# Kernel optimization log

Measured on AMD Instinct MI355X. Metric: run time of the kernel, lower is better.

Reference implementation:

```python
import jax, jax.numpy as jnp
import numpy as np

B, C_IN, C_OUT, H, W = 16, 192, 192, 128, 128
K_EXPERTS, LATENT_DIM = 8, 64


def setup_inputs() -> dict:
    key = jax.random.key(0)
    ks = jax.random.split(key, 6)
    s = lambda fan: np.float32(1.0 / np.sqrt(fan))
    return {
        "x": jax.random.normal(ks[0], (B, C_IN, H, W), jnp.float32),
        "latent": jax.random.normal(ks[1], (B, LATENT_DIM), jnp.float32),
        # DyConv2d: K expert 3x3 kernels + biases, attention FC from latent
        "expert_w": jax.random.normal(ks[2], (K_EXPERTS, C_OUT, C_IN, 3, 3), jnp.float32) * s(C_IN * 9),
        "expert_b": jnp.zeros((K_EXPERTS, C_OUT), jnp.float32),
        "attn_w": jax.random.normal(ks[3], (K_EXPERTS, LATENT_DIM), jnp.float32) * s(LATENT_DIM),
        "attn_b": jnp.zeros((K_EXPERTS,), jnp.float32),
        # static conv2 (3x3) weights
        "conv2_w": jax.random.normal(ks[4], (C_OUT, C_OUT, 3, 3), jnp.float32) * s(C_OUT * 9),
        "conv2_b": jnp.zeros((C_OUT,), jnp.float32),
    }


def _conv3x3(x, w, b):
    # x: [N,C,H,W], w: [O,I,3,3] -> [N,O,H,W]
    y = jax.lax.conv_general_dilated(
        x, w, window_strides=(1, 1), padding=((1, 1), (1, 1)),
        dimension_numbers=("NCHW", "OIHW", "NCHW"))
    return y + b[None, :, None, None]


def reference(x, latent, expert_w, expert_b, attn_w, attn_b, conv2_w, conv2_b):
    identity = x  # stride=1, in_ch==out_ch -> adaptor is None
    # ---- DyConv2d: latent -> expert attention -> per-sample kernel ----
    attn = jax.nn.softmax(latent @ attn_w.T + attn_b, axis=-1)        # [B,K]
    w_dyn = jnp.einsum("bk,koihw->boihw", attn, expert_w)            # [B,O,I,3,3]
    b_dyn = attn @ expert_b                                          # [B,O]
    # per-sample conv, vectorized over batch
    out = jax.vmap(lambda xi, wi, bi: _conv3x3(xi[None], wi, bi)[0])(x, w_dyn, b_dyn)
    out = jax.nn.silu(out)
    # ---- static conv3x3 ----
    out = _conv3x3(out, conv2_w, conv2_b)
    out = jax.nn.silu(out)
    return out + identity
```

## Files before the change

### kernel.cpp

```cpp
#include <hip/hip_runtime.h>
#include <stdint.h>

typedef __bf16 bf16;
typedef bf16 bf16x8 __attribute__((ext_vector_type(8)));
typedef bf16 bf16x4 __attribute__((ext_vector_type(4)));
typedef float f32x4 __attribute__((ext_vector_type(4)));

#define B_   16
#define CI   192
#define CO   192
#define H_   128
#define W_   128
#define KE   8
#define LD   64
#define KTOT 1728
#define HP   130
#define HPHP (HP*HP)
#define NPX  (H_*W_)
#define NT   54

__device__ __forceinline__ void gll16(const void* g, void* l) {
  __builtin_amdgcn_global_load_lds(
      (const __attribute__((address_space(1))) unsigned int*)g,
      (__attribute__((address_space(3))) unsigned int*)l, 16, 0, 0);
}

__device__ __forceinline__ float silu_f(float x) {
  return x / (1.f + __expf(-x));
}

__global__ void k_attn(const float* __restrict__ latent, const float* __restrict__ attn_w,
                       const float* __restrict__ attn_b, float* __restrict__ attn) {
  int t = threadIdx.x;
  int b = t >> 3, k = t & 7;
  float s = attn_b[k];
  for (int d = 0; d < LD; ++d) s += latent[b*LD + d] * attn_w[k*LD + d];
  float m = s;
  for (int off = 4; off; off >>= 1) m = fmaxf(m, __shfl_xor(m, off, 8));
  float e = __expf(s - m);
  float sum = e;
  for (int off = 4; off; off >>= 1) sum += __shfl_xor(sum, off, 8);
  attn[t] = e / sum;
}

__global__ void k_bdyn(const float* __restrict__ attn, const float* __restrict__ expert_b,
                       float* __restrict__ bdyn) {
  int j = blockIdx.x * 256 + threadIdx.x;
  if (j >= B_ * CO) return;
  int b = j / CO, o = j - b * CO;
  float s = 0.f;
  #pragma unroll
  for (int e = 0; e < KE; ++e) s += attn[b*KE + e] * expert_b[e*CO + o];
  bdyn[j] = s;
}

__global__ void k_wdyn(const float* __restrict__ expert_w, const float* __restrict__ attn,
                       bf16* __restrict__ w_re) {
  int o = blockIdx.x;
  int chunk = o >> 4, row = o & 15, c = (row >> 1) & 3;
  __shared__ float ew[KE][KTOT];
  __shared__ float al[B_][KE];
  for (int e = 0; e < KE; ++e)
    for (int j = threadIdx.x; j < KTOT; j += 256)
      ew[e][j] = expert_w[((size_t)e*CO + o)*KTOT + j];
  if (threadIdx.x < B_*KE) al[threadIdx.x >> 3][threadIdx.x & 7] = attn[threadIdx.x];
  __syncthreads();
  for (int idx = threadIdx.x; idx < B_*KTOT; idx += 256) {
    int b = idx / KTOT, k = idx - b*KTOT;
    int rs = k / 192, i = k - rs*192;
    float s = 0.f;
    #pragma unroll
    for (int e = 0; e < KE; ++e) s += al[b][e] * ew[e][i*9 + rs];
    int kt = k >> 5, kslot = (k >> 3) & 3, j = k & 7;
    int slot = row*4 + (kslot ^ c);
    w_re[((((size_t)b*NT + kt)*12 + chunk)*64 + slot)*8 + j] = (bf16)s;
  }
}

__global__ void k_w2re(const float* __restrict__ conv2_w, bf16* __restrict__ w2_re) {
  int o = blockIdx.x;
  int chunk = o >> 4, row = o & 15, c = (row >> 1) & 3;
  __shared__ float cw[KTOT];
  for (int j = threadIdx.x; j < KTOT; j += 256) cw[j] = conv2_w[(size_t)o*KTOT + j];
  __syncthreads();
  for (int k = threadIdx.x; k < KTOT; k += 256) {
    int rs = k / 192, i = k - rs*192;
    int kt = k >> 5, kslot = (k >> 3) & 3, j = k & 7;
    int slot = row*4 + (kslot ^ c);
    w2_re[(((size_t)kt*12 + chunk)*64 + slot)*8 + j] = (bf16)cw[i*9 + rs];
  }
}

__global__ void k_xpack(const float* __restrict__ x, bf16* __restrict__ xpack) {
  int h2 = blockIdx.x, ib = blockIdx.y, b = blockIdx.z;
  size_t rowbase = (((size_t)b*24 + ib)*HP + h2)*HP;
  int t = threadIdx.x;
  if (h2 == 0 || h2 == HP-1) {
    uint4 z = make_uint4(0,0,0,0);
    for (int w = t; w < HP; w += 128) *(uint4*)(xpack + (rowbase + w)*8) = z;
    return;
  }
  __shared__ float tt[8][128];
  int h = h2 - 1;
  #pragma unroll
  for (int ii = 0; ii < 8; ++ii)
    tt[ii][t] = x[(((size_t)b*CI + ib*8 + ii)*H_ + h)*W_ + t];
  __syncthreads();
  bf16x8 v;
  #pragma unroll
  for (int ii = 0; ii < 8; ++ii) v[ii] = (bf16)tt[ii][t];
  *(bf16x8*)(xpack + (rowbase + t + 1)*8) = v;
  if (t == 0) {
    uint4 z = make_uint4(0,0,0,0);
    *(uint4*)(xpack + rowbase*8) = z;
    *(uint4*)(xpack + (rowbase + HP-1)*8) = z;
  }
}

__global__ void k_midborder(bf16* __restrict__ midpack) {
  int bi = blockIdx.x;
  size_t base = (size_t)bi * HPHP;
  uint4 z = make_uint4(0,0,0,0);
  for (int j = threadIdx.x; j < 516; j += 256) {
    int h2, w2;
    if (j < 130)      { h2 = 0;       w2 = j; }
    else if (j < 260) { h2 = 129;     w2 = j - 130; }
    else if (j < 388) { h2 = j - 259; w2 = 0; }
    else              { h2 = j - 387; w2 = 129; }
    *(uint4*)(midpack + (base + (size_t)h2*HP + w2)*8) = z;
  }
}

template<int MODE>
__global__ __launch_bounds__(256, 2)
void k_conv(const bf16* __restrict__ wre, const bf16* __restrict__ inpack,
            const float* __restrict__ bias_g, const float* __restrict__ xin,
            bf16* __restrict__ outpack, float* __restrict__ outp) {
  const int tid  = threadIdx.x;
  const int lane = tid & 63;
  const int wv   = tid >> 6;
  const int wm   = wv >> 1;
  const int wn   = wv & 1;
  const int l15  = lane & 15, l4 = lane >> 4;

  const int bid  = blockIdx.x;
  const int n    = (bid & 7) * 128 + (bid >> 3);
  const int b    = n >> 6;
  const int tile = n & 63;
  const int p0   = tile * 256;
  const int h0   = tile * 2;

  __shared__ __align__(16) bf16 Alds[2][12*512];
  __shared__ __align__(16) bf16 Blds[3][16*512];
  __shared__ float bias_lds[CO];

  if (tid < CO) bias_lds[tid] = (MODE == 0) ? bias_g[b*CO + tid] : bias_g[tid];

  const size_t wbase = (MODE == 0) ? ((size_t)b*CO*KTOT) : 0;

  const bf16* aS = wre + wbase + (size_t)wv*512 + lane*8;
  const bf16* bS[4];
  #pragma unroll
  for (int c = 0; c < 4; ++c)
    bS[c] = inpack + ((((size_t)b*24 + wv)*HP + h0 + (c >> 1))*HP + (c & 1)*64 + lane)*8;

  int rsn = 0, ibn = 0, boff = 0;
  auto badv = [&]() {
    if (++ibn == 6) {
      ibn = 0; ++rsn;
      boff += (((rsn % 3) == 0) ? (HP - 2) : 1) * 8 - 20*HPHP*8;
    } else {
      boff += 4*HPHP*8;
    }
  };

  f32x4 acc[6][8];
  #pragma unroll
  for (int mf = 0; mf < 6; ++mf)
    #pragma unroll
    for (int nf = 0; nf < 8; ++nf)
      #pragma unroll
      for (int jj = 0; jj < 4; ++jj) acc[mf][nf][jj] = 0.f;

  const int sw = l15*4 + (l4 ^ ((l15 >> 1) & 3));

  {
    #pragma unroll
    for (int c = 0; c < 3; ++c) gll16(aS + c*2048, &Alds[0][(wv + c*4)*512]);
    aS += 6144;
    #pragma unroll
    for (int c = 0; c < 4; ++c) gll16(bS[c] + boff, &Blds[0][(wv*4 + c)*512]);
    badv();
    #pragma unroll
    for (int c = 0; c < 4; ++c) gll16(bS[c] + boff, &Blds[1][(wv*4 + c)*512]);
    badv();
  }

  int bcur = 0, bnxt = 2;
  for (int t = 0; t < NT; ++t) {
    if (t < NT-1) asm volatile("s_waitcnt vmcnt(4)" ::: "memory");
    else          asm volatile("s_waitcnt vmcnt(0)" ::: "memory");
    asm volatile("s_barrier" ::: "memory");

    const bf16* A  = Alds[t & 1];
    const bf16* Bp = Blds[bcur];

    bf16x8 af0 = *(const bf16x8*)(A + (wm*6 + 0)*512 + sw*8);
    bf16x8 af1 = *(const bf16x8*)(A + (wm*6 + 1)*512 + sw*8);
    bf16x8 af2 = *(const bf16x8*)(A + (wm*6 + 2)*512 + sw*8);
    bf16x8 af3 = *(const bf16x8*)(A + (wm*6 + 3)*512 + sw*8);
    bf16x8 af4 = *(const bf16x8*)(A + (wm*6 + 4)*512 + sw*8);
    bf16x8 af5 = *(const bf16x8*)(A + (wm*6 + 5)*512 + sw*8);

    if (t + 1 < NT) {
      bf16* An = (bf16*)Alds[(t+1) & 1];
      #pragma unroll
      for (int c = 0; c < 3; ++c) gll16(aS + c*2048, An + (wv + c*4)*512);
      aS += 6144;
    }
    if (t + 2 < NT) {
      bf16* Bn = (bf16*)Blds[bnxt];
      #pragma unroll
      for (int c = 0; c < 4; ++c) gll16(bS[c] + boff, Bn + (wv*4 + c)*512);
      badv();
    }

    __builtin_amdgcn_s_setprio(1);
    #pragma unroll
    for (int nf = 0; nf < 8; ++nf) {
      bf16x8 bv = *(const bf16x8*)(Bp + (size_t)(l4*256 + wn*128 + nf*16 + l15)*8);
      acc[0][nf] = __builtin_amdgcn_mfma_f32_16x16x32_bf16(af0, bv, acc[0][nf], 0, 0, 0);
      acc[1][nf] = __builtin_amdgcn_mfma_f32_16x16x32_bf16(af1, bv, acc[1][nf], 0, 0, 0);
      acc[2][nf] = __builtin_amdgcn_mfma_f32_16x16x32_bf16(af2, bv, acc[2][nf], 0, 0, 0);
      acc[3][nf] = __builtin_amdgcn_mfma_f32_16x16x32_bf16(af3, bv, acc[3][nf], 0, 0, 0);
      acc[4][nf] = __builtin_amdgcn_mfma_f32_16x16x32_bf16(af4, bv, acc[4][nf], 0, 0, 0);
      acc[5][nf] = __builtin_amdgcn_mfma_f32_16x16x32_bf16(af5, bv, acc[5][nf], 0, 0, 0);
    }
    __builtin_amdgcn_s_setprio(0);

    bcur = (bcur == 2) ? 0 : bcur + 1;
    bnxt = (bnxt == 2) ? 0 : bnxt + 1;
  }

  #pragma unroll
  for (int mf = 0; mf < 6; ++mf) {
    int ob = wm*96 + mf*16 + l4*4;
    #pragma unroll
    for (int nf = 0; nf < 8; ++nf) {
      int pl = wn*128 + nf*16 + l15;
      int p  = p0 + pl;
      f32x4 v = acc[mf][nf];
      if (MODE == 0) {
        int h = p >> 7, w = p & 127;
        bf16x4 pk;
        #pragma unroll
        for (int jj = 0; jj < 4; ++jj) {
          float xv = v[jj] + bias_lds[ob + jj];
          pk[jj] = (bf16)silu_f(xv);
        }
        size_t basep = (((size_t)b*24 + (ob >> 3))*HP + (h + 1))*HP + (w + 1);
        *(bf16x4*)(outpack + basep*8 + (ob & 7)) = pk;
      } else {
        #pragma unroll
        for (int jj = 0; jj < 4; ++jj) {
          float xv = silu_f(v[jj] + bias_lds[ob + jj]);
          size_t idx = ((size_t)b*CO + ob + jj)*NPX + p;
          outp[idx] = xv + xin[idx];
        }
      }
    }
  }
}

extern "C" void kernel_launch(void* const* d_in, const int* in_sizes, int n_in,
                              void* d_out, int out_size, void* d_ws, size_t ws_size,
                              hipStream_t stream) {
  const float* x        = (const float*)d_in[0];
  const float* latent   = (const float*)d_in[1];
  const float* expert_w = (const float*)d_in[2];
  const float* expert_b = (const float*)d_in[3];
  const float* attn_w   = (const float*)d_in[4];
  const float* attn_b   = (const float*)d_in[5];
  const float* conv2_w  = (const float*)d_in[6];
  const float* conv2_b  = (const float*)d_in[7];
  float* outp = (float*)d_out;

  char* base = (char*)d_ws;
  size_t off = 0;
  float* attn = (float*)(base + off); off += 4096;
  float* bdyn = (float*)(base + off); off += 16384;
  bf16* w_re  = (bf16*)(base + off);  off += (size_t)B_*CO*KTOT*2;
  bf16* w2_re = (bf16*)(base + off);  off += (size_t)CO*KTOT*2;
  bf16* xpack = (bf16*)(base + off);  off += (size_t)B_*24*HPHP*8*2;
  bf16* midpack = (bf16*)(base + off); off += (size_t)B_*24*HPHP*8*2;
  (void)ws_size; (void)in_sizes; (void)n_in; (void)out_size;

  k_attn<<<dim3(1), dim3(128), 0, stream>>>(latent, attn_w, attn_b, attn);
  k_bdyn<<<dim3(12), dim3(256), 0, stream>>>(attn, expert_b, bdyn);
  k_wdyn<<<dim3(CO), dim3(256), 0, stream>>>(expert_w, attn, w_re);
  k_w2re<<<dim3(CO), dim3(256), 0, stream>>>(conv2_w, w2_re);
  k_xpack<<<dim3(130, 24, 16), dim3(128), 0, stream>>>(x, xpack);
  k_midborder<<<dim3(B_*24), dim3(256), 0, stream>>>(midpack);
  k_conv<0><<<dim3(1024), dim3(256), 0, stream>>>(w_re, xpack, bdyn, x, midpack, outp);
  k_conv<1><<<dim3(1024), dim3(256), 0, stream>>>(w2_re, midpack, conv2_b, x, midpack, outp);
}
```

Measured before the change: 517.7 us.

## Reorder conv K loop to reuse input row window across horizontal taps

Reorders the packed weight K dimension so the horizontal kernel tap is innermost, letting one staged input row window in LDS serve three consecutive K steps with shifted reads. A-operand buffering becomes triple while B becomes double with a wider window, reducing global input loads per tile. The residual add in the second conv now reads the bf16 packed input instead of the fp32 original, saving bandwidth at the cost of residual precision.

```diff
diff --git a/kernel.cpp b/kernel.cpp
--- a/kernel.cpp
+++ b/kernel.cpp
@@ -1,5 +1,6 @@
 #include <hip/hip_runtime.h>
 #include <stdint.h>
+#include <stddef.h>
 
 typedef __bf16 bf16;
 typedef bf16 bf16x8 __attribute__((ext_vector_type(8)));
@@ -67,13 +68,15 @@
   __syncthreads();
   for (int idx = threadIdx.x; idx < B_*KTOT; idx += 256) {
     int b = idx / KTOT, k = idx - b*KTOT;
-    int rs = k / 192, i = k - rs*192;
-    float s = 0.f;
+    int kt = k >> 5, ks = (k >> 3) & 3, j = k & 7;
+    int r = kt / 18, t2 = kt - r*18;
+    int ibb = t2 / 3, s = t2 - ibb*3;
+    int i = ibb*32 + ks*8 + j;
+    float acc = 0.f;
     #pragma unroll
-    for (int e = 0; e < KE; ++e) s += al[b][e] * ew[e][i*9 + rs];
-    int kt = k >> 5, kslot = (k >> 3) & 3, j = k & 7;
-    int slot = row*4 + (kslot ^ c);
-    w_re[((((size_t)b*NT + kt)*12 + chunk)*64 + slot)*8 + j] = (bf16)s;
+    for (int e = 0; e < KE; ++e) acc += al[b][e] * ew[e][i*9 + r*3 + s];
+    int slot = row*4 + (ks ^ c);
+    w_re[((((size_t)b*NT + kt)*12 + chunk)*64 + slot)*8 + j] = (bf16)acc;
   }
 }
 
@@ -84,10 +87,12 @@
   for (int j = threadIdx.x; j < KTOT; j += 256) cw[j] = conv2_w[(size_t)o*KTOT + j];
   __syncthreads();
   for (int k = threadIdx.x; k < KTOT; k += 256) {
-    int rs = k / 192, i = k - rs*192;
-    int kt = k >> 5, kslot = (k >> 3) & 3, j = k & 7;
-    int slot = row*4 + (kslot ^ c);
-    w2_re[(((size_t)kt*12 + chunk)*64 + slot)*8 + j] = (bf16)cw[i*9 + rs];
+    int kt = k >> 5, ks = (k >> 3) & 3, j = k & 7;
+    int r = kt / 18, t2 = kt - r*18;
+    int ibb = t2 / 3, s = t2 - ibb*3;
+    int i = ibb*32 + ks*8 + j;
+    int slot = row*4 + (ks ^ c);
+    w2_re[(((size_t)kt*12 + chunk)*64 + slot)*8 + j] = (bf16)cw[i*9 + r*3 + s];
   }
 }
 
@@ -134,7 +139,7 @@
 template<int MODE>
 __global__ __launch_bounds__(256, 2)
 void k_conv(const bf16* __restrict__ wre, const bf16* __restrict__ inpack,
-            const float* __restrict__ bias_g, const float* __restrict__ xin,
+            const float* __restrict__ bias_g, const bf16* __restrict__ respack,
             bf16* __restrict__ outpack, float* __restrict__ outp) {
   const int tid  = threadIdx.x;
   const int lane = tid & 63;
@@ -150,8 +155,8 @@
   const int p0   = tile * 256;
   const int h0   = tile * 2;
 
-  __shared__ __align__(16) bf16 Alds[2][12*512];
-  __shared__ __align__(16) bf16 Blds[3][16*512];
+  __shared__ __align__(16) bf16 Alds[3][12*512];
+  __shared__ __align__(16) bf16 Blds[2][4*2560];
   __shared__ float bias_lds[CO];
 
   if (tid < CO) bias_lds[tid] = (MODE == 0) ? bias_g[b*CO + tid] : bias_g[tid];
@@ -159,19 +164,26 @@
   const size_t wbase = (MODE == 0) ? ((size_t)b*CO*KTOT) : 0;
 
   const bf16* aS = wre + wbase + (size_t)wv*512 + lane*8;
-  const bf16* bS[4];
-  #pragma unroll
-  for (int c = 0; c < 4; ++c)
-    bS[c] = inpack + ((((size_t)b*24 + wv)*HP + h0 + (c >> 1))*HP + (c & 1)*64 + lane)*8;
-
-  int rsn = 0, ibn = 0, boff = 0;
-  auto badv = [&]() {
-    if (++ibn == 6) {
-      ibn = 0; ++rsn;
-      boff += (((rsn % 3) == 0) ? (HP - 2) : 1) * 8 - 20*HPHP*8;
-    } else {
-      boff += 4*HPHP*8;
-    }
+  const bf16* bbase = inpack + (((size_t)b*24 + wv)*HPHP + (size_t)h0*HP)*8 + lane*8;
+  int ibm = 0; ptrdiff_t boffEl = 0;
+
+  auto stageA = [&](bf16* dbuf) {
+    bf16* d = dbuf + wv*512;
+    gll16(aS,        d);
+    gll16(aS + 2048, d + 2048);
+    gll16(aS + 4096, d + 4096);
+    aS += 6144;
+  };
+  auto stageB = [&](bf16* dbuf) {
+    const bf16* src = bbase + boffEl;
+    bf16* d = dbuf + wv*2560;
+    gll16(src,        d);
+    gll16(src +  512, d +  512);
+    gll16(src + 1024, d + 1024);
+    gll16(src + 1536, d + 1536);
+    gll16(src + 1568, d + 1568);
+    if (++ibm == 6) { ibm = 0; boffEl += (ptrdiff_t)(HP - 20*HPHP)*8; }
+    else boffEl += (ptrdiff_t)4*HPHP*8;
   };
 
   f32x4 acc[6][8];
@@ -183,63 +195,52 @@
       for (int jj = 0; jj < 4; ++jj) acc[mf][nf][jj] = 0.f;
 
   const int sw = l15*4 + (l4 ^ ((l15 >> 1) & 3));
-
-  {
+  const int bvb = l4*2560 + (wn*130 + l15)*8;
+
+  stageA(Alds[0]);
+  stageA(Alds[1]);
+  stageB(Blds[0]);
+
+  bf16* Bcur = (bf16*)Blds[0];
+  bf16* Bnxt = (bf16*)Blds[1];
+
+  for (int m = 0; m < 18; ++m) {
     #pragma unroll
-    for (int c = 0; c < 3; ++c) gll16(aS + c*2048, &Alds[0][(wv + c*4)*512]);
-    aS += 6144;
-    #pragma unroll
-    for (int c = 0; c < 4; ++c) gll16(bS[c] + boff, &Blds[0][(wv*4 + c)*512]);
-    badv();
-    #pragma unroll
-    for (int c = 0; c < 4; ++c) gll16(bS[c] + boff, &Blds[1][(wv*4 + c)*512]);
-    badv();
-  }
-
-  int bcur = 0, bnxt = 2;
-  for (int t = 0; t < NT; ++t) {
-    if (t < NT-1) asm volatile("s_waitcnt vmcnt(4)" ::: "memory");
-    else          asm volatile("s_waitcnt vmcnt(0)" ::: "memory");
-    asm volatile("s_barrier" ::: "memory");
-
-    const bf16* A  = Alds[t & 1];
-    const bf16* Bp = Blds[bcur];
-
-    bf16x8 af0 = *(const bf16x8*)(A + (wm*6 + 0)*512 + sw*8);
-    bf16x8 af1 = *(const bf16x8*)(A + (wm*6 + 1)*512 + sw*8);
-    bf16x8 af2 = *(const bf16x8*)(A + (wm*6 + 2)*512 + sw*8);
-    bf16x8 af3 = *(const bf16x8*)(A + (wm*6 + 3)*512 + sw*8);
-    bf16x8 af4 = *(const bf16x8*)(A + (wm*6 + 4)*512 + sw*8);
-    bf16x8 af5 = *(const bf16x8*)(A + (wm*6 + 5)*512 + sw*8);
-
-    if (t + 1 < NT) {
-      bf16* An = (bf16*)Alds[(t+1) & 1];
+    for (int s = 0; s < 3; ++s) {
+      if (s == 2) {
+        if (m == 17) asm volatile("s_waitcnt vmcnt(0)" ::: "memory");
+        else         asm volatile("s_waitcnt vmcnt(8)" ::: "memory");
+      } else {
+        asm volatile("s_waitcnt vmcnt(3)" ::: "memory");
+      }
+      asm volatile("s_barrier" ::: "memory");
+
+      const bf16* A = Alds[s];
+      bf16x8 af0 = *(const bf16x8*)(A + (wm*6 + 0)*512 + sw*8);
+      bf16x8 af1 = *(const bf16x8*)(A + (wm*6 + 1)*512 + sw*8);
+      bf16x8 af2 = *(const bf16x8*)(A + (wm*6 + 2)*512 + sw*8);
+      bf16x8 af3 = *(const bf16x8*)(A + (wm*6 + 3)*512 + sw*8);
+      bf16x8 af4 = *(const bf16x8*)(A + (wm*6 + 4)*512 + sw*8);
+      bf16x8 af5 = *(const bf16x8*)(A + (wm*6 + 5)*512 + sw*8);
+
+      if (3*m + s + 2 < NT) stageA(Alds[(s+2)%3]);
+      if (s == 1 && m < 17) stageB(Bnxt);
+
+      const bf16* bp = Bcur + bvb + s*8;
+      __builtin_amdgcn_s_setprio(1);
       #pragma unroll
-      for (int c = 0; c < 3; ++c) gll16(aS + c*2048, An + (wv + c*4)*512);
-      aS += 6144;
+      for (int nf = 0; nf < 8; ++nf) {
+        bf16x8 bv = *(const bf16x8*)(bp + nf*128);
+        acc[0][nf] = __builtin_amdgcn_mfma_f32_16x16x32_bf16(af0, bv, acc[0][nf], 0, 0, 0);
+        acc[1][nf] = __builtin_amdgcn_mfma_f32_16x16x32_bf16(af1, bv, acc[1][nf], 0, 0, 0);
+        acc[2][nf] = __builtin_amdgcn_mfma_f32_16x16x32_bf16(af2, bv, acc[2][nf], 0, 0, 0);
+        acc[3][nf] = __builtin_amdgcn_mfma_f32_16x16x32_bf16(af3, bv, acc[3][nf], 0, 0, 0);
+        acc[4][nf] = __builtin_amdgcn_mfma_f32_16x16x32_bf16(af4, bv, acc[4][nf], 0, 0, 0);
+        acc[5][nf] = __builtin_amdgcn_mfma_f32_16x16x32_bf16(af5, bv, acc[5][nf], 0, 0, 0);
+      }
+      __builtin_amdgcn_s_setprio(0);
     }
-    if (t + 2 < NT) {
-      bf16* Bn = (bf16*)Blds[bnxt];
-      #pragma unroll
-      for (int c = 0; c < 4; ++c) gll16(bS[c] + boff, Bn + (wv*4 + c)*512);
-      badv();
-    }
-
-    __builtin_amdgcn_s_setprio(1);
-    #pragma unroll
-    for (int nf = 0; nf < 8; ++nf) {
-      bf16x8 bv = *(const bf16x8*)(Bp + (size_t)(l4*256 + wn*128 + nf*16 + l15)*8);
-      acc[0][nf] = __builtin_amdgcn_mfma_f32_16x16x32_bf16(af0, bv, acc[0][nf], 0, 0, 0);
-      acc[1][nf] = __builtin_amdgcn_mfma_f32_16x16x32_bf16(af1, bv, acc[1][nf], 0, 0, 0);
-      acc[2][nf] = __builtin_amdgcn_mfma_f32_16x16x32_bf16(af2, bv, acc[2][nf], 0, 0, 0);
-      acc[3][nf] = __builtin_amdgcn_mfma_f32_16x16x32_bf16(af3, bv, acc[3][nf], 0, 0, 0);
-      acc[4][nf] = __builtin_amdgcn_mfma_f32_16x16x32_bf16(af4, bv, acc[4][nf], 0, 0, 0);
-      acc[5][nf] = __builtin_amdgcn_mfma_f32_16x16x32_bf16(af5, bv, acc[5][nf], 0, 0, 0);
-    }
-    __builtin_amdgcn_s_setprio(0);
-
-    bcur = (bcur == 2) ? 0 : bcur + 1;
-    bnxt = (bnxt == 2) ? 0 : bnxt + 1;
+    { bf16* t = Bcur; Bcur = Bnxt; Bnxt = t; }
   }
 
   #pragma unroll
@@ -250,22 +251,23 @@
       int pl = wn*128 + nf*16 + l15;
       int p  = p0 + pl;
       f32x4 v = acc[mf][nf];
+      int h = p >> 7, w = p & 127;
+      size_t basep = (((size_t)b*24 + (ob >> 3))*HP + (h + 1))*HP + (w + 1);
       if (MODE == 0) {
-        int h = p >> 7, w = p & 127;
         bf16x4 pk;
         #pragma unroll
         for (int jj = 0; jj < 4; ++jj) {
           float xv = v[jj] + bias_lds[ob + jj];
           pk[jj] = (bf16)silu_f(xv);
         }
-        size_t basep = (((size_t)b*24 + (ob >> 3))*HP + (h + 1))*HP + (w + 1);
         *(bf16x4*)(outpack + basep*8 + (ob & 7)) = pk;
       } else {
+        bf16x4 rr = *(const bf16x4*)(respack + basep*8 + (ob & 7));
         #pragma unroll
         for (int jj = 0; jj < 4; ++jj) {
           float xv = silu_f(v[jj] + bias_lds[ob + jj]);
           size_t idx = ((size_t)b*CO + ob + jj)*NPX + p;
-          outp[idx] = xv + xin[idx];
+          outp[idx] = xv + (float)rr[jj];
         }
       }
     }
@@ -301,6 +303,6 @@
   k_w2re<<<dim3(CO), dim3(256), 0, stream>>>(conv2_w, w2_re);
   k_xpack<<<dim3(130, 24, 16), dim3(128), 0, stream>>>(x, xpack);
   k_midborder<<<dim3(B_*24), dim3(256), 0, stream>>>(midpack);
-  k_conv<0><<<dim3(1024), dim3(256), 0, stream>>>(w_re, xpack, bdyn, x, midpack, outp);
-  k_conv<1><<<dim3(1024), dim3(256), 0, stream>>>(w2_re, midpack, conv2_b, x, midpack, outp);
-}
+  k_conv<0><<<dim3(1024), dim3(256), 0, stream>>>(w_re, xpack, bdyn, xpack, midpack, outp);
+  k_conv<1><<<dim3(1024), dim3(256), 0, stream>>>(w2_re, midpack, conv2_b, xpack, midpack, outp);
+}
```

Result: faster. 501.4 us (-3.2%).
